# Kernel optimization log

Hardware: AMD Instinct MI355X
Metric: run time of the kernel (lower is better)

Reference implementation:

```python
import jax, jax.numpy as jnp
import numpy as np

N_EMBED = 1024
NUM_EXPERTS = 8
TOP_K = 2


def setup_inputs() -> dict:
    key = jax.random.key(0)
    ks = jax.random.split(key, 7)
    d, e, h = N_EMBED, NUM_EXPERTS, 4 * N_EMBED
    s = 1.0 / np.sqrt(d)
    sh = 1.0 / np.sqrt(h)
    return {
        "x": jax.random.normal(ks[0], (4, 2048, d), dtype=jnp.float32),
        "Wg": jax.random.uniform(ks[1], (d, e), jnp.float32, -s, s),
        "bg": jax.random.uniform(ks[2], (e,), jnp.float32, -s, s),
        "W1": jax.random.uniform(ks[3], (e, d, h), jnp.float32, -s, s),
        "b1": jax.random.uniform(ks[4], (e, h), jnp.float32, -s, s),
        "W2": jax.random.uniform(ks[5], (e, h, d), jnp.float32, -sh, sh),
        "b2": jax.random.uniform(ks[6], (e, d), jnp.float32, -sh, sh),
    }


def reference(x, Wg, bg, W1, b1, W2, b2):
    # Gating: softmax over ALL experts, then top-k (no renormalization, matching original)
    logits = jnp.einsum("bsd,de->bse", x, Wg) + bg
    probs = jax.nn.softmax(logits, axis=-1)
    weights, indices = jax.lax.top_k(probs, TOP_K)  # [B,S,K]

    out = jnp.zeros_like(x)
    for ei in range(NUM_EXPERTS):
        # combined gate weight for this expert per token [B,S]
        gate = jnp.sum(jnp.where(indices == ei, weights, 0.0), axis=-1)
        hid = jax.nn.relu(jnp.einsum("bsd,dh->bsh", x, W1[ei]) + b1[ei])
        eo = jnp.einsum("bsh,hd->bsd", hid, W2[ei]) + b2[ei]
        out = out + gate[..., None] * eo
    return out
```

## Files before the change

### kernel.cpp

```cpp
#include <hip/hip_runtime.h>
#include <hip/hip_bf16.h>
#include <stdint.h>
#include <math.h>


#define TOKENS   8192
#define DIM      1024
#define HIDN     4096
#define NEXP     8
#define PAIRS    (TOKENS * 2)
#define MAXROWS  (PAIRS + NEXP * 64)
#define MAXTILES 136
#define NHB      128

typedef __attribute__((ext_vector_type(8))) short short8;
typedef __attribute__((ext_vector_type(4))) float f32x4;

#define AS1 __attribute__((address_space(1)))
#define AS3 __attribute__((address_space(3)))

__device__ inline short bf16b(float f) {
    __hip_bfloat16 h = __float2bfloat16(f);
    return *reinterpret_cast<short*>(&h);
}

__global__ __launch_bounds__(256) void gating_kernel(
    const float* __restrict__ x, const float* __restrict__ Wg,
    const float* __restrict__ bg,
    int* __restrict__ topk_e, float* __restrict__ topk_w)
{
    int t    = blockIdx.x * 4 + (threadIdx.x >> 6);
    int lane = threadIdx.x & 63;
    if (t >= TOKENS) return;
    const float* xr = x + (size_t)t * DIM;

    float acc[8];
#pragma unroll
    for (int e = 0; e < 8; ++e) acc[e] = 0.f;

#pragma unroll 4
    for (int j = 0; j < DIM / 64; ++j) {
        int idx = j * 64 + lane;
        float xv = xr[idx];
        const float* wr = Wg + (size_t)idx * 8;
        float4 w0 = *(const float4*)(wr);
        float4 w1 = *(const float4*)(wr + 4);
        acc[0] += xv * w0.x; acc[1] += xv * w0.y;
        acc[2] += xv * w0.z; acc[3] += xv * w0.w;
        acc[4] += xv * w1.x; acc[5] += xv * w1.y;
        acc[6] += xv * w1.z; acc[7] += xv * w1.w;
    }
#pragma unroll
    for (int off = 32; off > 0; off >>= 1)
#pragma unroll
        for (int e = 0; e < 8; ++e) acc[e] += __shfl_down(acc[e], off);

    if (lane == 0) {
        float lg[8];
#pragma unroll
        for (int e = 0; e < 8; ++e) lg[e] = acc[e] + bg[e];
        float mx = lg[0];
#pragma unroll
        for (int e = 1; e < 8; ++e) mx = fmaxf(mx, lg[e]);
        float p[8]; float s = 0.f;
#pragma unroll
        for (int e = 0; e < 8; ++e) { p[e] = expf(lg[e] - mx); s += p[e]; }
        int e0 = 0;
#pragma unroll
        for (int e = 1; e < 8; ++e) if (p[e] > p[e0]) e0 = e;
        int e1 = -1;
#pragma unroll
        for (int e = 0; e < 8; ++e)
            if (e != e0 && (e1 < 0 || p[e] > p[e1])) e1 = e;
        float inv = 1.f / s;
        topk_e[t * 2 + 0] = e0;  topk_w[t * 2 + 0] = p[e0] * inv;
        topk_e[t * 2 + 1] = e1;  topk_w[t * 2 + 1] = p[e1] * inv;
    }
}

__global__ __launch_bounds__(128) void hist_kernel(
    const int* __restrict__ topk_e, int* __restrict__ hist)
{
    __shared__ int h[8];
    int t = threadIdx.x, b = blockIdx.x;
    if (t < 8) h[t] = 0;
    __syncthreads();
    atomicAdd(&h[topk_e[b * 128 + t]], 1);
    __syncthreads();
    if (t < 8) hist[b * 8 + t] = h[t];
}

__global__ __launch_bounds__(128) void plan_kernel(
    const int* __restrict__ hist, int* __restrict__ base,
    int* __restrict__ tile_e, int* __restrict__ tile_row0, int* __restrict__ n_tiles)
{
    __shared__ int sx[8][NHB];
    __shared__ int tot[8];
    __shared__ int segs[8];
    __shared__ int wtot[2];
    int t = threadIdx.x, lane = t & 63, wid = t >> 6;
#pragma unroll
    for (int e = 0; e < 8; ++e) {
        int hv = hist[t * 8 + e];
        int v = hv;
#pragma unroll
        for (int off = 1; off < 64; off <<= 1) {
            int n = __shfl_up(v, off);
            if (lane >= off) v += n;
        }
        if (lane == 63) wtot[wid] = v;
        __syncthreads();
        int incl = v + (wid ? wtot[0] : 0);
        sx[e][t] = incl - hv;
        if (t == NHB - 1) tot[e] = incl;
        __syncthreads();
    }
    if (t == 0) {
        int off = 0, nt = 0;
        for (int e = 0; e < 8; ++e) {
            segs[e] = off;
            int tl = (tot[e] + 127) >> 7;
            for (int i = 0; i < tl; ++i) { tile_e[nt] = e; tile_row0[nt] = off + i * 128; ++nt; }
            off += tl * 128;
        }
        *n_tiles = nt;
    }
    __syncthreads();
#pragma unroll
    for (int e = 0; e < 8; ++e) base[t * 8 + e] = segs[e] + sx[e][t];
}

__global__ __launch_bounds__(128) void gather_rank(
    const int* __restrict__ topk_e, const float* __restrict__ topk_w,
    const int* __restrict__ base, int* __restrict__ pair_row,
    int* __restrict__ row_token, float* __restrict__ row_gate)
{
    __shared__ int cnt[8];
    int t = threadIdx.x, b = blockIdx.x;
    if (t < 8) cnt[t] = 0;
    __syncthreads();
    int pr = b * 128 + t;
    int e  = topk_e[pr];
    int lr = atomicAdd(&cnt[e], 1);
    int row = base[b * 8 + e] + lr;
    pair_row[pr]   = row;
    row_token[row] = pr >> 1;
    row_gate[row]  = topk_w[pr];
}

__global__ __launch_bounds__(256) void scatter_copy(
    const float* __restrict__ x, const int* __restrict__ pair_row,
    __hip_bfloat16* __restrict__ xe)
{
    int b = blockIdx.x;
    int wv = threadIdx.x >> 6, lane = threadIdx.x & 63;
#pragma unroll 4
    for (int i = 0; i < 16; ++i) {
        int p   = b * 64 + i * 4 + wv;
        int row = pair_row[p];
        int tok = p >> 1;
        const float* xr = x + (size_t)tok * DIM;
        __hip_bfloat16* xo = xe + (size_t)row * DIM;
        int idx = lane * 16;
        float4 v0 = *(const float4*)(xr + idx);
        float4 v1 = *(const float4*)(xr + idx + 4);
        float4 v2 = *(const float4*)(xr + idx + 8);
        float4 v3 = *(const float4*)(xr + idx + 12);
        short8 o0, o1;
        o0[0] = bf16b(v0.x); o0[1] = bf16b(v0.y); o0[2] = bf16b(v0.z); o0[3] = bf16b(v0.w);
        o0[4] = bf16b(v1.x); o0[5] = bf16b(v1.y); o0[6] = bf16b(v1.z); o0[7] = bf16b(v1.w);
        o1[0] = bf16b(v2.x); o1[1] = bf16b(v2.y); o1[2] = bf16b(v2.z); o1[3] = bf16b(v2.w);
        o1[4] = bf16b(v3.x); o1[5] = bf16b(v3.y); o1[6] = bf16b(v3.z); o1[7] = bf16b(v3.w);
        *(short8*)(xo + idx)     = o0;
        *(short8*)(xo + idx + 8) = o1;
    }
}

__global__ __launch_bounds__(256) void transpose_cvt_kernel(
    const float* __restrict__ src, __hip_bfloat16* __restrict__ dst,
    int rows, int cols)
{
    __shared__ float tile[32][33];
    int e  = blockIdx.z;
    const float* s = src + (size_t)e * rows * cols;
    __hip_bfloat16* d = dst + (size_t)e * rows * cols;
    int c0 = blockIdx.x * 32, r0 = blockIdx.y * 32;
    int tx = threadIdx.x & 31, ty = threadIdx.x >> 5;
#pragma unroll
    for (int j = 0; j < 4; ++j) {
        int rr = ty + j * 8;
        tile[rr][tx] = s[(size_t)(r0 + rr) * cols + c0 + tx];
    }
    __syncthreads();
    int t  = threadIdx.x;
    int cr = t >> 3;
    int g  = t & 7;
    ushort o[4];
#pragma unroll
    for (int j = 0; j < 4; ++j) o[j] = (ushort)bf16b(tile[g * 4 + j][cr]);
    *(uint2*)(d + (size_t)(c0 + cr) * rows + r0 + g * 4) = *(uint2*)o;
}

template <int MODE>
__global__ __launch_bounds__(256) void moe_gemm(
    const __hip_bfloat16* __restrict__ A,
    const __hip_bfloat16* __restrict__ Bw,
    const float* __restrict__ bias,
    const int* __restrict__ tile_e, const int* __restrict__ tile_row0,
    const int* __restrict__ n_tiles,
    int K, int N,
    __hip_bfloat16* __restrict__ hid,
    const int* __restrict__ row_token, const float* __restrict__ row_gate,
    float* __restrict__ out)
{
    int tidx = blockIdx.x;
    if (tidx >= *n_tiles) return;
    int e  = tile_e[tidx];
    int m0 = tile_row0[tidx];
    int n0 = blockIdx.y * 128;
    const __hip_bfloat16* Bb = Bw + (size_t)e * N * K;

    __shared__ __hip_bfloat16 lA[2][128 * 64];
    __shared__ __hip_bfloat16 lB[2][128 * 64];

    int tid  = threadIdx.x;
    int w    = tid >> 6;
    int l    = tid & 63;
    int r    = l & 15;
    int quad = l >> 4;
    int subrow = l >> 3;
    int cswz   = ((l & 7) ^ subrow) * 16;
    int wm = (w >> 1) * 64;
    int wn = (w & 1) * 64;

    const f32x4 fzero = {0.f, 0.f, 0.f, 0.f};
    f32x4 acc[4][4];
#pragma unroll
    for (int mi = 0; mi < 4; ++mi)
#pragma unroll
        for (int ni = 0; ni < 4; ++ni) acc[mi][ni] = fzero;

    const size_t ldb = (size_t)K * 2;
    int rsw = (r & 7);

    auto STAGE = [&](int buf, int k0) {
#pragma unroll
        for (int i = 0; i < 4; ++i) {
            int chunk = i * 4 + w;
            int rowA  = chunk * 8 + subrow;
            const char* gA = (const char*)A + (size_t)(m0 + rowA) * ldb + (size_t)k0 * 2 + cswz;
            const char* gB = (const char*)Bb + (size_t)(n0 + rowA) * ldb + (size_t)k0 * 2 + cswz;
            char* sA = (char*)(&lA[buf][0]) + chunk * 1024;
            char* sB = (char*)(&lB[buf][0]) + chunk * 1024;
            __builtin_amdgcn_global_load_lds((const AS1 void*)gA, (AS3 void*)sA, 16, 0, 0);
            __builtin_amdgcn_global_load_lds((const AS1 void*)gB, (AS3 void*)sB, 16, 0, 0);
        }
    };

    STAGE(0, 0);

    int cur = 0;
    for (int k0 = 0; k0 < K; k0 += 64, cur ^= 1) {
        int knext = k0 + 64;
        if (knext < K) {
            STAGE(cur ^ 1, knext);
            asm volatile("s_waitcnt vmcnt(8)" ::: "memory");
        } else {
            asm volatile("s_waitcnt vmcnt(0)" ::: "memory");
        }
        __builtin_amdgcn_s_barrier();

#pragma unroll
        for (int kk = 0; kk < 2; ++kk) {
            int slot = ((kk * 4 + quad) ^ rsw) * 16;
            short8 aF[4], bF[4];
#pragma unroll
            for (int mi = 0; mi < 4; ++mi) {
                int row = wm + mi * 16 + r;
                aF[mi] = *(const short8*)((const char*)&lA[cur][0] + row * 128 + slot);
            }
#pragma unroll
            for (int ni = 0; ni < 4; ++ni) {
                int row = wn + ni * 16 + r;
                bF[ni] = *(const short8*)((const char*)&lB[cur][0] + row * 128 + slot);
            }
#pragma unroll
            for (int mi = 0; mi < 4; ++mi)
#pragma unroll
                for (int ni = 0; ni < 4; ++ni)
                    acc[mi][ni] = __builtin_amdgcn_mfma_f32_16x16x32_bf16(
                        aF[mi], bF[ni], acc[mi][ni], 0, 0, 0);
        }
        __builtin_amdgcn_s_barrier();
    }

    if (MODE == 1) {
#pragma unroll
        for (int mi = 0; mi < 4; ++mi)
#pragma unroll
            for (int i = 0; i < 4; ++i) {
                int row = m0 + wm + mi * 16 + quad * 4 + i;
                size_t rb = (size_t)row * N;
#pragma unroll
                for (int ni = 0; ni < 4; ++ni) {
                    int col = n0 + wn + ni * 16 + r;
                    float v = acc[mi][ni][i] + bias[e * N + col];
                    hid[rb + col] = __float2bfloat16(fmaxf(v, 0.f));
                }
            }
    } else {
#pragma unroll
        for (int mi = 0; mi < 4; ++mi)
#pragma unroll
            for (int i = 0; i < 4; ++i) {
                int row = m0 + wm + mi * 16 + quad * 4 + i;
                int token = row_token[row];
                if ((unsigned)token < (unsigned)TOKENS) {
                    float g = row_gate[row];
                    float* orow = out + (size_t)token * DIM;
#pragma unroll
                    for (int ni = 0; ni < 4; ++ni) {
                        int col = n0 + wn + ni * 16 + r;
                        float v = acc[mi][ni][i] + bias[e * N + col];
                        atomicAdd(orow + col, g * v);
                    }
                }
            }
    }
}

extern "C" void kernel_launch(void* const* d_in, const int* in_sizes, int n_in,
                              void* d_out, int out_size, void* d_ws, size_t ws_size,
                              hipStream_t stream) {
    const float* x  = (const float*)d_in[0];
    const float* Wg = (const float*)d_in[1];
    const float* bg = (const float*)d_in[2];
    const float* W1 = (const float*)d_in[3];
    const float* b1 = (const float*)d_in[4];
    const float* W2 = (const float*)d_in[5];
    const float* b2 = (const float*)d_in[6];
    float* out = (float*)d_out;

    char* w = (char*)d_ws;
    int*   n_tiles   = (int*)(w + 0);
    int*   tile_e    = (int*)(w + 256);
    int*   tile_row0 = (int*)(w + 2048);
    int*   hist      = (int*)(w + 4096);
    int*   base      = (int*)(w + 8192);
    int*   topk_e    = (int*)(w + 12288);
    float* topk_w    = (float*)(w + 77824);
    int*   pair_row  = (int*)(w + 143360);
    int*   row_token = (int*)(w + 208896);
    float* row_gate  = (float*)(w + 278528);
    __hip_bfloat16* xe  = (__hip_bfloat16*)(w + 348160);
    __hip_bfloat16* hid = (__hip_bfloat16*)(w + 35999744ULL);
    __hip_bfloat16* W1b = (__hip_bfloat16*)(w + 178606080ULL);
    __hip_bfloat16* W2b = (__hip_bfloat16*)(w + 245714944ULL);

    hipMemsetAsync(out, 0, (size_t)out_size * sizeof(float), stream);

    gating_kernel<<<TOKENS / 4, 256, 0, stream>>>(x, Wg, bg, topk_e, topk_w);
    hist_kernel<<<NHB, 128, 0, stream>>>(topk_e, hist);
    plan_kernel<<<1, 128, 0, stream>>>(hist, base, tile_e, tile_row0, n_tiles);
    gather_rank<<<NHB, 128, 0, stream>>>(topk_e, topk_w, base, pair_row,
                                         row_token, row_gate);
    scatter_copy<<<256, 256, 0, stream>>>(x, pair_row, xe);

    transpose_cvt_kernel<<<dim3(HIDN / 32, DIM / 32, NEXP), 256, 0, stream>>>(W1, W1b, DIM, HIDN);
    transpose_cvt_kernel<<<dim3(DIM / 32, HIDN / 32, NEXP), 256, 0, stream>>>(W2, W2b, HIDN, DIM);

    moe_gemm<1><<<dim3(MAXTILES, HIDN / 128), 256, 0, stream>>>(
        xe, W1b, b1, tile_e, tile_row0, n_tiles, DIM, HIDN,
        hid, nullptr, nullptr, nullptr);
    moe_gemm<2><<<dim3(MAXTILES, DIM / 128), 256, 0, stream>>>(
        hid, W2b, b2, tile_e, tile_row0, n_tiles, HIDN, DIM,
        nullptr, row_token, row_gate, out);
}
```

Before: 946.1 us.

## Use 256x256 MoE GEMM tiles with 8 waves, split-K for down projection

The grouped expert GEMMs now use 256x256 output tiles computed by 512-thread blocks (8 waves, each 128x64), which raises arithmetic intensity per LDS load. The main loop is restructured with interleaved prefetch, barriers and s_setprio around MFMA bursts, and tile indices are remapped across blocks. Partial tiles are tracked with a per-tile valid count, and the second GEMM is split along K into two slices that both accumulate through atomics, with the bias added only by the first slice. The cost is extra memsets of the expert buffer, twice the atomic traffic in the output stage, and some padding waste from the larger tiles.

```diff
diff --git a/kernel.cpp b/kernel.cpp
--- a/kernel.cpp
+++ b/kernel.cpp
@@ -9,8 +9,8 @@
 #define HIDN     4096
 #define NEXP     8
 #define PAIRS    (TOKENS * 2)
-#define MAXROWS  (PAIRS + NEXP * 64)
-#define MAXTILES 136
+#define ROWCAP   17408
+#define MAXT256  72
 #define NHB      128
 
 typedef __attribute__((ext_vector_type(8))) short short8;
@@ -92,7 +92,8 @@
 
 __global__ __launch_bounds__(128) void plan_kernel(
     const int* __restrict__ hist, int* __restrict__ base,
-    int* __restrict__ tile_e, int* __restrict__ tile_row0, int* __restrict__ n_tiles)
+    int* __restrict__ tile_e, int* __restrict__ tile_row0,
+    int* __restrict__ tile_valid, int* __restrict__ n_tiles)
 {
     __shared__ int sx[8][NHB];
     __shared__ int tot[8];
@@ -119,9 +120,16 @@
         int off = 0, nt = 0;
         for (int e = 0; e < 8; ++e) {
             segs[e] = off;
-            int tl = (tot[e] + 127) >> 7;
-            for (int i = 0; i < tl; ++i) { tile_e[nt] = e; tile_row0[nt] = off + i * 128; ++nt; }
-            off += tl * 128;
+            int len = ((tot[e] + 127) >> 7) << 7;
+            int tl  = (len + 255) >> 8;
+            for (int i = 0; i < tl; ++i) {
+                tile_e[nt]     = e;
+                tile_row0[nt]  = off + i * 256;
+                int v          = len - i * 256;
+                tile_valid[nt] = v > 256 ? 256 : v;
+                ++nt;
+            }
+            off += len;
         }
         *n_tiles = nt;
     }
@@ -202,26 +210,32 @@
 }
 
 template <int MODE>
-__global__ __launch_bounds__(256) void moe_gemm(
+__global__ __launch_bounds__(512, 2) void moe_gemm(
     const __hip_bfloat16* __restrict__ A,
     const __hip_bfloat16* __restrict__ Bw,
     const float* __restrict__ bias,
     const int* __restrict__ tile_e, const int* __restrict__ tile_row0,
-    const int* __restrict__ n_tiles,
+    const int* __restrict__ tile_valid, const int* __restrict__ n_tiles,
     int K, int N,
     __hip_bfloat16* __restrict__ hid,
     const int* __restrict__ row_token, const float* __restrict__ row_gate,
     float* __restrict__ out)
 {
-    int tidx = blockIdx.x;
+    int bx   = blockIdx.x;
+    int tidx = (bx & 7) * (MAXT256 / 8) + (bx >> 3);
     if (tidx >= *n_tiles) return;
-    int e  = tile_e[tidx];
-    int m0 = tile_row0[tidx];
-    int n0 = blockIdx.y * 128;
-    const __hip_bfloat16* Bb = Bw + (size_t)e * N * K;
-
-    __shared__ __hip_bfloat16 lA[2][128 * 64];
-    __shared__ __hip_bfloat16 lB[2][128 * 64];
+    int e     = tile_e[tidx];
+    int m0    = tile_row0[tidx];
+    int valid = tile_valid[tidx];
+    int n0    = blockIdx.y * 256;
+    const char* Ab = (const char*)A;
+    const char* Bb = (const char*)(Bw + (size_t)e * N * K);
+
+    int klen  = K / (int)gridDim.z;
+    int kbase = blockIdx.z * klen;
+    int nkt   = klen >> 6;
+
+    __shared__ __hip_bfloat16 lds[2][4][8192];
 
     int tid  = threadIdx.x;
     int w    = tid >> 6;
@@ -230,102 +244,137 @@
     int quad = l >> 4;
     int subrow = l >> 3;
     int cswz   = ((l & 7) ^ subrow) * 16;
-    int wm = (w >> 1) * 64;
-    int wn = (w & 1) * 64;
+    int rsw    = r & 7;
+    int wm = (w >> 2) * 128;
+    int wn = (w & 3) * 64;
+    int aPart = wm >> 7;
+    int bPart = 2 + (wn >> 7);
+    int bColBase = wn & 64;
+
+    const size_t ldb = (size_t)K * 2;
 
     const f32x4 fzero = {0.f, 0.f, 0.f, 0.f};
-    f32x4 acc[4][4];
-#pragma unroll
-    for (int mi = 0; mi < 4; ++mi)
-#pragma unroll
-        for (int ni = 0; ni < 4; ++ni) acc[mi][ni] = fzero;
-
-    const size_t ldb = (size_t)K * 2;
-    int rsw = (r & 7);
-
-    auto STAGE = [&](int buf, int k0) {
-#pragma unroll
-        for (int i = 0; i < 4; ++i) {
-            int chunk = i * 4 + w;
-            int rowA  = chunk * 8 + subrow;
-            const char* gA = (const char*)A + (size_t)(m0 + rowA) * ldb + (size_t)k0 * 2 + cswz;
-            const char* gB = (const char*)Bb + (size_t)(n0 + rowA) * ldb + (size_t)k0 * 2 + cswz;
-            char* sA = (char*)(&lA[buf][0]) + chunk * 1024;
-            char* sB = (char*)(&lB[buf][0]) + chunk * 1024;
-            __builtin_amdgcn_global_load_lds((const AS1 void*)gA, (AS3 void*)sA, 16, 0, 0);
-            __builtin_amdgcn_global_load_lds((const AS1 void*)gB, (AS3 void*)sB, 16, 0, 0);
+    f32x4 acc[8][4];
+#pragma unroll
+    for (int fr = 0; fr < 8; ++fr)
+#pragma unroll
+        for (int fc = 0; fc < 4; ++fc) acc[fr][fc] = fzero;
+
+    auto STAGE = [&](int buf, int P, int k0) {
+#pragma unroll
+        for (int j = 0; j < 2; ++j) {
+            int rloc = j * 64 + w * 8 + subrow;
+            int rabs;
+            const char* src;
+            if (P < 2) {
+                rabs = m0 + P * 128 + rloc;
+                rabs = rabs < (ROWCAP - 1) ? rabs : (ROWCAP - 1);
+                src  = Ab;
+            } else {
+                rabs = n0 + (P - 2) * 128 + rloc;
+                src  = Bb;
+            }
+            const char* g = src + (size_t)rabs * ldb + (size_t)k0 * 2 + cswz;
+            char* d = (char*)(&lds[buf][P][0]) + j * 8192 + w * 1024;
+            __builtin_amdgcn_global_load_lds((const AS1 void*)g, (AS3 void*)d, 16, 0, 0);
         }
     };
 
-    STAGE(0, 0);
-
-    int cur = 0;
-    for (int k0 = 0; k0 < K; k0 += 64, cur ^= 1) {
-        int knext = k0 + 64;
-        if (knext < K) {
-            STAGE(cur ^ 1, knext);
-            asm volatile("s_waitcnt vmcnt(8)" ::: "memory");
-        } else {
-            asm volatile("s_waitcnt vmcnt(0)" ::: "memory");
-        }
-        __builtin_amdgcn_s_barrier();
-
-#pragma unroll
-        for (int kk = 0; kk < 2; ++kk) {
-            int slot = ((kk * 4 + quad) ^ rsw) * 16;
-            short8 aF[4], bF[4];
-#pragma unroll
-            for (int mi = 0; mi < 4; ++mi) {
-                int row = wm + mi * 16 + r;
-                aF[mi] = *(const short8*)((const char*)&lA[cur][0] + row * 128 + slot);
-            }
-#pragma unroll
-            for (int ni = 0; ni < 4; ++ni) {
-                int row = wn + ni * 16 + r;
-                bF[ni] = *(const short8*)((const char*)&lB[cur][0] + row * 128 + slot);
-            }
-#pragma unroll
-            for (int mi = 0; mi < 4; ++mi)
-#pragma unroll
-                for (int ni = 0; ni < 4; ++ni)
-                    acc[mi][ni] = __builtin_amdgcn_mfma_f32_16x16x32_bf16(
-                        aF[mi], bF[ni], acc[mi][ni], 0, 0, 0);
-        }
-        __builtin_amdgcn_s_barrier();
+    STAGE(0, 0, kbase); STAGE(0, 1, kbase); STAGE(0, 2, kbase); STAGE(0, 3, kbase);
+    asm volatile("s_waitcnt vmcnt(0)" ::: "memory");
+    __builtin_amdgcn_s_barrier();
+
+    for (int t = 0; t < nkt; ++t) {
+        int buf = t & 1;
+        int kn  = kbase + ((t + 1) << 6);
+        bool pre = (t + 1 < nkt);
+        const char* ldsA = (const char*)&lds[buf][aPart][0];
+        const char* ldsB = (const char*)&lds[buf][bPart][0];
+        short8 bF[4][2];
+#pragma unroll
+        for (int p = 0; p < 4; ++p) {
+            if (p == 0) {
+#pragma unroll
+                for (int fc = 0; fc < 4; ++fc)
+#pragma unroll
+                    for (int kk = 0; kk < 2; ++kk)
+                        bF[fc][kk] = *(const short8*)(ldsB
+                            + (bColBase + fc * 16 + r) * 128
+                            + (((kk * 4 + quad) ^ rsw) * 16));
+            }
+            short8 aF[2][2];
+#pragma unroll
+            for (int fi = 0; fi < 2; ++fi)
+#pragma unroll
+                for (int kk = 0; kk < 2; ++kk)
+                    aF[fi][kk] = *(const short8*)(ldsA
+                        + ((p * 2 + fi) * 16 + r) * 128
+                        + (((kk * 4 + quad) ^ rsw) * 16));
+            if (pre) {
+                if (p == 0) { STAGE(buf ^ 1, 0, kn); STAGE(buf ^ 1, 1, kn); }
+                if (p == 1) { STAGE(buf ^ 1, 2, kn); STAGE(buf ^ 1, 3, kn); }
+            }
+            __builtin_amdgcn_s_barrier();
+            __builtin_amdgcn_s_setprio(1);
+#pragma unroll
+            for (int fi = 0; fi < 2; ++fi)
+#pragma unroll
+                for (int fc = 0; fc < 4; ++fc)
+#pragma unroll
+                    for (int kk = 0; kk < 2; ++kk)
+                        acc[p * 2 + fi][fc] = __builtin_amdgcn_mfma_f32_16x16x32_bf16(
+                            aF[fi][kk], bF[fc][kk], acc[p * 2 + fi][fc], 0, 0, 0);
+            __builtin_amdgcn_s_setprio(0);
+            if (p == 3) {
+                if (pre) asm volatile("s_waitcnt vmcnt(0)" ::: "memory");
+                __builtin_amdgcn_s_barrier();
+                __builtin_amdgcn_sched_barrier(0);
+            } else {
+                __builtin_amdgcn_s_barrier();
+            }
+        }
     }
 
     if (MODE == 1) {
 #pragma unroll
-        for (int mi = 0; mi < 4; ++mi)
+        for (int fr = 0; fr < 8; ++fr) {
+            int lrow = wm + fr * 16 + quad * 4;
 #pragma unroll
             for (int i = 0; i < 4; ++i) {
-                int row = m0 + wm + mi * 16 + quad * 4 + i;
-                size_t rb = (size_t)row * N;
-#pragma unroll
-                for (int ni = 0; ni < 4; ++ni) {
-                    int col = n0 + wn + ni * 16 + r;
-                    float v = acc[mi][ni][i] + bias[e * N + col];
-                    hid[rb + col] = __float2bfloat16(fmaxf(v, 0.f));
-                }
-            }
-    } else {
-#pragma unroll
-        for (int mi = 0; mi < 4; ++mi)
-#pragma unroll
-            for (int i = 0; i < 4; ++i) {
-                int row = m0 + wm + mi * 16 + quad * 4 + i;
-                int token = row_token[row];
-                if ((unsigned)token < (unsigned)TOKENS) {
-                    float g = row_gate[row];
-                    float* orow = out + (size_t)token * DIM;
-#pragma unroll
-                    for (int ni = 0; ni < 4; ++ni) {
-                        int col = n0 + wn + ni * 16 + r;
-                        float v = acc[mi][ni][i] + bias[e * N + col];
-                        atomicAdd(orow + col, g * v);
+                if (lrow + i < valid) {
+                    size_t rb = (size_t)(m0 + lrow + i) * N;
+#pragma unroll
+                    for (int fc = 0; fc < 4; ++fc) {
+                        int col = n0 + wn + fc * 16 + r;
+                        float v = acc[fr][fc][i] + bias[e * N + col];
+                        hid[rb + col] = __float2bfloat16(fmaxf(v, 0.f));
                     }
                 }
             }
+        }
+    } else {
+        bool addb = (blockIdx.z == 0);
+#pragma unroll
+        for (int fr = 0; fr < 8; ++fr) {
+            int lrow = wm + fr * 16 + quad * 4;
+#pragma unroll
+            for (int i = 0; i < 4; ++i) {
+                int row = m0 + lrow + i;
+                if (lrow + i < valid) {
+                    int token = row_token[row];
+                    if ((unsigned)token < (unsigned)TOKENS) {
+                        float g = row_gate[row];
+                        float* orow = out + (size_t)token * DIM;
+#pragma unroll
+                        for (int fc = 0; fc < 4; ++fc) {
+                            int col = n0 + wn + fc * 16 + r;
+                            float v = acc[fr][fc][i] + (addb ? bias[e * N + col] : 0.f);
+                            atomicAdd(orow + col, g * v);
+                        }
+                    }
+                }
+            }
+        }
     }
 }
 
@@ -342,26 +391,30 @@
     float* out = (float*)d_out;
 
     char* w = (char*)d_ws;
-    int*   n_tiles   = (int*)(w + 0);
-    int*   tile_e    = (int*)(w + 256);
-    int*   tile_row0 = (int*)(w + 2048);
-    int*   hist      = (int*)(w + 4096);
-    int*   base      = (int*)(w + 8192);
-    int*   topk_e    = (int*)(w + 12288);
-    float* topk_w    = (float*)(w + 77824);
-    int*   pair_row  = (int*)(w + 143360);
-    int*   row_token = (int*)(w + 208896);
-    float* row_gate  = (float*)(w + 278528);
+    int*   n_tiles    = (int*)(w + 0);
+    int*   tile_e     = (int*)(w + 256);
+    int*   tile_valid = (int*)(w + 1024);
+    int*   tile_row0  = (int*)(w + 2048);
+    int*   hist       = (int*)(w + 4096);
+    int*   base       = (int*)(w + 8192);
+    int*   topk_e     = (int*)(w + 12288);
+    float* topk_w     = (float*)(w + 77824);
+    int*   pair_row   = (int*)(w + 143360);
+    int*   row_token  = (int*)(w + 208896);
+    float* row_gate   = (float*)(w + 278528);
     __hip_bfloat16* xe  = (__hip_bfloat16*)(w + 348160);
     __hip_bfloat16* hid = (__hip_bfloat16*)(w + 35999744ULL);
     __hip_bfloat16* W1b = (__hip_bfloat16*)(w + 178606080ULL);
     __hip_bfloat16* W2b = (__hip_bfloat16*)(w + 245714944ULL);
 
     hipMemsetAsync(out, 0, (size_t)out_size * sizeof(float), stream);
+    hipMemsetAsync(row_token, 0xFF, 69632, stream);
+    hipMemsetAsync(row_gate, 0, 69632, stream);
+    hipMemsetAsync(xe, 0, 35651584ULL, stream);
 
     gating_kernel<<<TOKENS / 4, 256, 0, stream>>>(x, Wg, bg, topk_e, topk_w);
     hist_kernel<<<NHB, 128, 0, stream>>>(topk_e, hist);
-    plan_kernel<<<1, 128, 0, stream>>>(hist, base, tile_e, tile_row0, n_tiles);
+    plan_kernel<<<1, 128, 0, stream>>>(hist, base, tile_e, tile_row0, tile_valid, n_tiles);
     gather_rank<<<NHB, 128, 0, stream>>>(topk_e, topk_w, base, pair_row,
                                          row_token, row_gate);
     scatter_copy<<<256, 256, 0, stream>>>(x, pair_row, xe);
@@ -369,10 +422,10 @@
     transpose_cvt_kernel<<<dim3(HIDN / 32, DIM / 32, NEXP), 256, 0, stream>>>(W1, W1b, DIM, HIDN);
     transpose_cvt_kernel<<<dim3(DIM / 32, HIDN / 32, NEXP), 256, 0, stream>>>(W2, W2b, HIDN, DIM);
 
-    moe_gemm<1><<<dim3(MAXTILES, HIDN / 128), 256, 0, stream>>>(
-        xe, W1b, b1, tile_e, tile_row0, n_tiles, DIM, HIDN,
+    moe_gemm<1><<<dim3(MAXT256, HIDN / 256, 1), 512, 0, stream>>>(
+        xe, W1b, b1, tile_e, tile_row0, tile_valid, n_tiles, DIM, HIDN,
         hid, nullptr, nullptr, nullptr);
-    moe_gemm<2><<<dim3(MAXTILES, DIM / 128), 256, 0, stream>>>(
-        hid, W2b, b2, tile_e, tile_row0, n_tiles, HIDN, DIM,
+    moe_gemm<2><<<dim3(MAXT256, DIM / 256, 2), 512, 0, stream>>>(
+        hid, W2b, b2, tile_e, tile_row0, tile_valid, n_tiles, HIDN, DIM,
         nullptr, row_token, row_gate, out);
 }
```

After: 921.9 us. -2.6%, faster.
